# Optimization experiments

Measured on AMD Instinct MI355X. Metric: run time of the kernel, lower is better.

The kernel has to match this reference:

```python
import jax, jax.numpy as jnp
import numpy as np

DIM = 768
HEADS = 12
N_PATCH = 1024
ORDER = 5
DECAY = 0.5
EPS = 1e-6


def _exact_mask(N, order, decay):
    # 2D grid graph adjacency, row-major node order (matches sorted nx.grid_2d_graph nodes)
    side = int(np.sqrt(N))
    A = np.zeros((N, N), dtype=np.float64)
    idx = np.arange(N)
    r, c = idx // side, idx % side
    right = idx[c < side - 1]
    A[right, right + 1] = 1.0
    A[right + 1, right] = 1.0
    down = idx[r < side - 1]
    A[down, down + side] = 1.0
    A[down + side, down] = 1.0
    D_inv = 1.0 / np.maximum(A.sum(axis=1), 1.0)
    W = D_inv[:, None] * A
    M = np.eye(N)
    W_k = np.eye(N)
    coeff = 1.0
    for _ in range(order):
        W_k = W_k @ W
        coeff *= decay
        M += coeff * W_k
    M = M / M.sum(axis=1, keepdims=True)
    return jnp.asarray(M, dtype=jnp.float32)


def setup_inputs() -> dict:
    key = jax.random.key(0)
    k1, k2, k3, k4 = jax.random.split(key, 4)
    B = 4
    x = jax.random.normal(k1, (B, N_PATCH, DIM), dtype=jnp.float32)
    # nn.Linear(dim, 3*dim, bias=False): store as [dim, 3*dim] for x @ W
    scale = 1.0 / np.sqrt(DIM)
    W_qkv = jax.random.uniform(k2, (DIM, 3 * DIM), dtype=jnp.float32, minval=-scale, maxval=scale)
    W_out = jax.random.uniform(k3, (DIM, DIM), dtype=jnp.float32, minval=-scale, maxval=scale)
    b_out = jax.random.uniform(k4, (DIM,), dtype=jnp.float32, minval=-scale, maxval=scale)
    mask = _exact_mask(N_PATCH, ORDER, DECAY)
    return {"x": x, "W_qkv": W_qkv, "W_out": W_out, "b_out": b_out, "mask": mask}


def reference(x, W_qkv, W_out, b_out, mask):
    B, N, C = x.shape
    H, D = HEADS, C // HEADS
    qkv = x @ W_qkv  # [B, N, 3C]
    q, k, v = jnp.split(qkv, 3, axis=-1)
    # [B, N, C] -> [B, H, N, D]
    q, k, v = (t.reshape(B, N, H, D).transpose(0, 2, 1, 3) for t in (q, k, v))
    # feature map
    q = jax.nn.relu(q) + EPS
    k = jax.nn.relu(k) + EPS
    # (q^T @ M)^T = M^T @ q  ->  einsum over node axis
    q_graph = jnp.einsum('nm,bhnd->bhmd', mask, q)
    k_graph = jnp.einsum('nm,bhnd->bhmd', mask, k)
    q = q + 0.1 * q_graph
    k = k + 0.1 * k_graph
    linear_kernel = jnp.einsum('bhnd,bhmd->bhnm', q, k)  # [B, H, N, N]
    masked_kernel = linear_kernel * mask[None, None, :, :]
    z = 1.0 / (masked_kernel.sum(axis=-1, keepdims=True) + EPS)  # [B, H, N, 1]
    out = jnp.einsum('bhnm,bhmd->bhnd', masked_kernel, v) * z
    out = out.transpose(0, 2, 1, 3).reshape(B, N, C)
    return out @ W_out + b_out
```

## Files before the change

### kernel.cpp

```cpp
#include <hip/hip_runtime.h>

#define NP   1024
#define DIM  768
#define NH   12
#define HD   64
#define TQ   2304
#define EPS  1e-6f

typedef __attribute__((ext_vector_type(8))) short bf16x8;
typedef __attribute__((ext_vector_type(4))) float f32x4;

#define MFMA(a, b, c) __builtin_amdgcn_mfma_f32_16x16x32_bf16((a), (b), (c), 0, 0, 0)

__device__ __forceinline__ unsigned short f2b(float x) {
    unsigned int u = __builtin_bit_cast(unsigned int, x);
    u = (u + 0x7fffu + ((u >> 16) & 1u)) >> 16;
    return (unsigned short)u;
}
__device__ __forceinline__ float b2f(unsigned short h) {
    unsigned int u = ((unsigned int)h) << 16;
    return __builtin_bit_cast(float, u);
}
#if __has_builtin(__builtin_amdgcn_cvt_pk_bf16_f32)
typedef __attribute__((ext_vector_type(2))) __bf16 bf16x2t;
__device__ __forceinline__ unsigned int pk2(float lo, float hi) {
    bf16x2t v = __builtin_amdgcn_cvt_pk_bf16_f32(lo, hi);
    return __builtin_bit_cast(unsigned int, v);
}
#else
__device__ __forceinline__ unsigned int pk2(float lo, float hi) {
    return (unsigned int)f2b(lo) | ((unsigned int)f2b(hi) << 16);
}
#endif
__device__ __forceinline__ void gld16(const void* g, void* l) {
    __builtin_amdgcn_global_load_lds((const __attribute__((address_space(1))) unsigned int*)g,
                                     (__attribute__((address_space(3))) unsigned int*)l,
                                     16, 0, 0);
}

__global__ __launch_bounds__(256) void k_prep(const float* __restrict__ W_qkv,
                                              const float* __restrict__ W_out,
                                              const float* __restrict__ mask,
                                              unsigned short* __restrict__ WqkvT,
                                              unsigned short* __restrict__ WoutT,
                                              unsigned short* __restrict__ M2) {
    __shared__ float buf[64][65];
    const int bx = blockIdx.x, t = threadIdx.x;
    const float* in; unsigned short* outp; int R, C, ct, rt; bool isMask = false;
    if (bx < 432)      { int q = bx;       in = W_qkv; outp = WqkvT; R = 768;  C = 2304; ct = q % 36; rt = q / 36; }
    else if (bx < 576) { int q = bx - 432; in = W_out; outp = WoutT; R = 768;  C = 768;  ct = q % 12; rt = q / 12; }
    else               { int q = bx - 576; in = mask;  outp = M2;    R = 1024; C = 1024; ct = q % 16; rt = q / 16; isMask = true; }
    const int r0 = rt * 64, c0 = ct * 64;
    const int rr = t >> 4, cc = (t & 15) * 4;
    #pragma unroll
    for (int p = 0; p < 4; ++p) {
        float4 v = *(const float4*)(in + (size_t)(r0 + p * 16 + rr) * C + c0 + cc);
        buf[p * 16 + rr][cc + 0] = v.x; buf[p * 16 + rr][cc + 1] = v.y;
        buf[p * 16 + rr][cc + 2] = v.z; buf[p * 16 + rr][cc + 3] = v.w;
    }
    __syncthreads();
    const int oc = t >> 2, orr = (t & 3) * 16;
    alignas(16) unsigned short tmp[16];
    if (isMask) {
        #pragma unroll
        for (int j = 0; j < 16; ++j) {
            float v = 0.1f * buf[orr + j][oc] + ((c0 + oc) == (r0 + orr + j) ? 1.f : 0.f);
            tmp[j] = f2b(v);
        }
    } else {
        #pragma unroll
        for (int j = 0; j < 16; ++j) tmp[j] = f2b(buf[orr + j][oc]);
    }
    unsigned short* dst = outp + (size_t)(c0 + oc) * R + r0 + orr;
    *(uint4*)dst = *(const uint4*)tmp;
    *(uint4*)(dst + 8) = *(const uint4*)(tmp + 8);
}

__global__ __launch_bounds__(512) void k_gemm1(const float* __restrict__ X,
                                               const unsigned short* __restrict__ Bt,
                                               unsigned short* __restrict__ T) {
    __shared__ unsigned short As[2][128][32];
    __shared__ unsigned short Bs[2][128][32];
    const int tid = threadIdx.x, w = tid >> 6, l = tid & 63;
    const int bid = blockIdx.x;
    const int mstrip = (bid & 7) * 4 + ((bid >> 3) & 3);
    const int nstrip = bid >> 5;
    const int m0 = mstrip * 128, n0 = nstrip * 128;
    const int wm = (w & 3) * 32, wn = (w >> 2) * 64;
    const int quad = l >> 4, col = l & 15;
    const int lr = l >> 2, lc = (l & 3) * 8;
    const int arow = tid >> 2, akc = (tid & 3) * 8;

    f32x4 acc[2][4] = {};
    for (int k0 = 0; k0 < DIM; k0 += 64) {
        #pragma unroll
        for (int hh = 0; hh < 2; ++hh) {
            gld16(Bt + (size_t)(n0 + w * 16 + lr) * DIM + k0 + hh * 32 + lc, &Bs[hh][w * 16][0]);
            const float* xp = X + (size_t)(m0 + arow) * DIM + k0 + hh * 32 + akc;
            float4 xa = *(const float4*)xp;
            float4 xb = *(const float4*)(xp + 4);
            uint4 o;
            o.x = pk2(xa.x, xa.y); o.y = pk2(xa.z, xa.w);
            o.z = pk2(xb.x, xb.y); o.w = pk2(xb.z, xb.w);
            *(uint4*)&As[hh][arow][akc] = o;
        }
        __syncthreads();
        #pragma unroll
        for (int hh = 0; hh < 2; ++hh) {
            bf16x8 a[2], b[4];
            #pragma unroll
            for (int i = 0; i < 2; ++i) a[i] = *(const bf16x8*)&As[hh][wm + i * 16 + col][quad * 8];
            #pragma unroll
            for (int j = 0; j < 4; ++j) b[j] = *(const bf16x8*)&Bs[hh][wn + j * 16 + col][quad * 8];
            #pragma unroll
            for (int i = 0; i < 2; ++i)
                #pragma unroll
                for (int j = 0; j < 4; ++j)
                    acc[i][j] = MFMA(a[i], b[j], acc[i][j]);
        }
        __syncthreads();
    }

    const int cgb = n0 + wn;
    const int slot = cgb / DIM;
    const int h = (cgb % DIM) >> 6;
    const bool act = (slot < 2);
    const int sh = slot * 48 + (m0 >> 10) * NH + h;
    const int npb = (m0 & 1023) + wm + quad * 4;
    #pragma unroll
    for (int j = 0; j < 4; ++j) {
        unsigned short* dcol = T + ((size_t)(sh * HD + j * 16 + col)) * NP + npb;
        #pragma unroll
        for (int i = 0; i < 2; ++i) {
            float v0 = acc[i][j][0], v1 = acc[i][j][1], v2 = acc[i][j][2], v3 = acc[i][j][3];
            if (act) {
                v0 = fmaxf(v0, 0.f) + EPS; v1 = fmaxf(v1, 0.f) + EPS;
                v2 = fmaxf(v2, 0.f) + EPS; v3 = fmaxf(v3, 0.f) + EPS;
            }
            uint2 o; o.x = pk2(v0, v1); o.y = pk2(v2, v3);
            *(uint2*)(dcol + i * 16) = o;
        }
    }
}

__global__ __launch_bounds__(256) void k_graphmix(const unsigned short* __restrict__ M2,
                                                  const unsigned short* __restrict__ T,
                                                  unsigned short* __restrict__ q2) {
    const int bh = blockIdx.y, mt = blockIdx.x;
    const int m0 = mt * 64;
    __shared__ unsigned short M2s[4][64][32], Fq[4][64][32], Fk[4][64][32];
    const int tid = threadIdx.x, w = tid >> 6, l = tid & 63;
    const int quad = l >> 4, col = l & 15;
    const int lr = l >> 2, lc = (l & 3) * 8;
    const unsigned short* Tq = T + (size_t)bh * HD * NP;
    const unsigned short* Tk = T + (size_t)(48 + bh) * HD * NP;

    f32x4 accq[4] = {}, acck[4] = {};
    const int nr0 = min(max(2 * mt - 5, 0), 20) * 32;
    for (int it = 0; it < 3; ++it) {
        const int nc = nr0 + it * 128;
        __syncthreads();
        #pragma unroll
        for (int hh = 0; hh < 4; ++hh) {
            gld16(M2 + (size_t)(m0 + w * 16 + lr) * NP + nc + hh * 32 + lc, &M2s[hh][w * 16][0]);
            gld16(Tq + (size_t)(w * 16 + lr) * NP + nc + hh * 32 + lc, &Fq[hh][w * 16][0]);
            gld16(Tk + (size_t)(w * 16 + lr) * NP + nc + hh * 32 + lc, &Fk[hh][w * 16][0]);
        }
        __syncthreads();
        #pragma unroll
        for (int ks = 0; ks < 4; ++ks) {
            bf16x8 bm = *(const bf16x8*)&M2s[ks][w * 16 + col][quad * 8];
            #pragma unroll
            for (int dt = 0; dt < 4; ++dt) {
                bf16x8 aq = *(const bf16x8*)&Fq[ks][dt * 16 + col][quad * 8];
                bf16x8 ak = *(const bf16x8*)&Fk[ks][dt * 16 + col][quad * 8];
                accq[dt] = MFMA(aq, bm, accq[dt]);
                acck[dt] = MFMA(ak, bm, acck[dt]);
            }
        }
    }
    unsigned short* q2q = q2 + ((size_t)bh * NP + m0 + w * 16 + col) * HD;
    unsigned short* q2k = q2 + ((size_t)(48 + bh) * NP + m0 + w * 16 + col) * HD;
    #pragma unroll
    for (int dt = 0; dt < 4; ++dt) {
        const int d0 = dt * 16 + quad * 4;
        uint2 oq; oq.x = pk2(accq[dt][0], accq[dt][1]); oq.y = pk2(accq[dt][2], accq[dt][3]);
        uint2 ok; ok.x = pk2(acck[dt][0], acck[dt][1]); ok.y = pk2(acck[dt][2], acck[dt][3]);
        *(uint2*)(q2q + d0) = oq;
        *(uint2*)(q2k + d0) = ok;
    }
}

__global__ __launch_bounds__(256) void k_attn(const unsigned short* __restrict__ q2,
                                              const unsigned short* __restrict__ T,
                                              const float* __restrict__ mask,
                                              unsigned short* __restrict__ attnb) {
    const int bh = blockIdx.y, b = bh / NH, h = bh % NH;
    const int nt = blockIdx.x, n0 = nt * 64;
    __shared__ unsigned short Qs[2][64][32];
    __shared__ unsigned short Ks[2][64][32];
    __shared__ unsigned short VT[2][64][32];
    __shared__ unsigned int Ss2[32][68];
    __shared__ float rowz[64];
    const int tid = threadIdx.x, w = tid >> 6, l = tid & 63;
    const int quad = l >> 4, col = l & 15;
    const int lr = l >> 2, lc = (l & 3) * 8;

    const unsigned short* qb = q2 + ((size_t)bh * NP + n0) * HD;
    const unsigned short* kb = q2 + (size_t)(48 + bh) * NP * HD;
    const unsigned short* vtb = T + (size_t)(96 + bh) * HD * NP;

    #pragma unroll
    for (int hh = 0; hh < 2; ++hh)
        gld16(qb + (size_t)(w * 16 + lr) * HD + hh * 32 + lc, &Qs[hh][w * 16][0]);

    f32x4 oacc[4] = {};
    float racc[4] = {};
    const int mr0 = min(max(2 * nt - 5, 0), 20) * 32;
    const unsigned int sel = (col & 1) ? 0x07060302u : 0x05040100u;

    for (int it = 0; it < 6; ++it) {
        const int m0 = mr0 + it * 64;
        __syncthreads();
        #pragma unroll
        for (int hh = 0; hh < 2; ++hh) {
            gld16(kb + (size_t)(m0 + w * 16 + lr) * HD + hh * 32 + lc, &Ks[hh][w * 16][0]);
            gld16(vtb + (size_t)(w * 16 + lr) * NP + m0 + hh * 32 + lc, &VT[hh][w * 16][0]);
        }
        float mreg[4][4];
        #pragma unroll
        for (int mtt = 0; mtt < 4; ++mtt)
            #pragma unroll
            for (int r = 0; r < 4; ++r)
                mreg[mtt][r] = mask[(size_t)(n0 + w * 16 + quad * 4 + r) * NP
                                    + m0 + mtt * 16 + col];
        __syncthreads();

        f32x4 s[4] = {};
        #pragma unroll
        for (int ks = 0; ks < 2; ++ks) {
            bf16x8 aq = *(const bf16x8*)&Qs[ks][w * 16 + col][quad * 8];
            #pragma unroll
            for (int mtt = 0; mtt < 4; ++mtt) {
                bf16x8 bk = *(const bf16x8*)&Ks[ks][mtt * 16 + col][quad * 8];
                s[mtt] = MFMA(aq, bk, s[mtt]);
            }
        }
        {
            const int npr = w * 8 + quad * 2;
            #pragma unroll
            for (int mtt = 0; mtt < 4; ++mtt) {
                float v0 = s[mtt][0] * mreg[mtt][0];
                float v1 = s[mtt][1] * mreg[mtt][1];
                float v2 = s[mtt][2] * mreg[mtt][2];
                float v3 = s[mtt][3] * mreg[mtt][3];
                racc[0] += v0; racc[1] += v1; racc[2] += v2; racc[3] += v3;
                Ss2[npr][mtt * 16 + col]     = pk2(v0, v1);
                Ss2[npr + 1][mtt * 16 + col] = pk2(v2, v3);
            }
        }
        __syncthreads();
        #pragma unroll
        for (int ks = 0; ks < 2; ++ks) {
            const unsigned int* rp = &Ss2[w * 8 + (col >> 1)][ks * 32 + quad * 8];
            uint4 U  = *(const uint4*)rp;
            uint4 U2 = *(const uint4*)(rp + 4);
            uint4 fr;
            fr.x = __builtin_amdgcn_perm(U.y,  U.x,  sel);
            fr.y = __builtin_amdgcn_perm(U.w,  U.z,  sel);
            fr.z = __builtin_amdgcn_perm(U2.y, U2.x, sel);
            fr.w = __builtin_amdgcn_perm(U2.w, U2.z, sel);
            bf16x8 as = __builtin_bit_cast(bf16x8, fr);
            #pragma unroll
            for (int dt = 0; dt < 4; ++dt) {
                bf16x8 bv = *(const bf16x8*)&VT[ks][dt * 16 + col][quad * 8];
                oacc[dt] = MFMA(as, bv, oacc[dt]);
            }
        }
    }

    #pragma unroll
    for (int r = 0; r < 4; ++r) {
        float v = racc[r];
        v += __shfl_xor(v, 1); v += __shfl_xor(v, 2);
        v += __shfl_xor(v, 4); v += __shfl_xor(v, 8);
        if (col == 0) rowz[w * 16 + quad * 4 + r] = v;
    }
    __syncthreads();
    #pragma unroll
    for (int r = 0; r < 4; ++r) {
        const int nl = w * 16 + quad * 4 + r;
        const float z = 1.f / (rowz[nl] + EPS);
        #pragma unroll
        for (int dt = 0; dt < 4; ++dt)
            attnb[(size_t)(b * NP + n0 + nl) * DIM + h * HD + dt * 16 + col] =
                f2b(oacc[dt][r] * z);
    }
}

__global__ __launch_bounds__(256) void k_gemm2(const unsigned short* __restrict__ A,
                                               const unsigned short* __restrict__ Bt,
                                               const float* __restrict__ bias,
                                               float* __restrict__ C) {
    __shared__ unsigned short As[2][64][32];
    __shared__ unsigned short Bs[2][64][32];
    const int tid = threadIdx.x, w = tid >> 6, l = tid & 63;
    const int bid = blockIdx.x;
    const int mstrip = (bid & 7) * 8 + ((bid >> 3) & 7);
    const int nstrip = bid >> 6;
    const int m0 = mstrip * 64, n0 = nstrip * 64;
    const int wm = (w & 1) * 32, wn = (w >> 1) * 32;
    const int quad = l >> 4, col = l & 15;
    const int lr = l >> 2, lc = (l & 3) * 8;

    f32x4 acc[2][2] = {};
    for (int k0 = 0; k0 < DIM; k0 += 64) {
        #pragma unroll
        for (int hh = 0; hh < 2; ++hh) {
            gld16(A + (size_t)(m0 + w * 16 + lr) * DIM + k0 + hh * 32 + lc, &As[hh][w * 16][0]);
            gld16(Bt + (size_t)(n0 + w * 16 + lr) * DIM + k0 + hh * 32 + lc, &Bs[hh][w * 16][0]);
        }
        __syncthreads();
        #pragma unroll
        for (int hh = 0; hh < 2; ++hh) {
            bf16x8 a[2], b[2];
            #pragma unroll
            for (int i = 0; i < 2; ++i) a[i] = *(const bf16x8*)&As[hh][wm + i * 16 + col][quad * 8];
            #pragma unroll
            for (int j = 0; j < 2; ++j) b[j] = *(const bf16x8*)&Bs[hh][wn + j * 16 + col][quad * 8];
            #pragma unroll
            for (int i = 0; i < 2; ++i)
                #pragma unroll
                for (int j = 0; j < 2; ++j)
                    acc[i][j] = MFMA(a[i], b[j], acc[i][j]);
        }
        __syncthreads();
    }
    #pragma unroll
    for (int i = 0; i < 2; ++i)
        #pragma unroll
        for (int j = 0; j < 2; ++j) {
            const int n = n0 + wn + j * 16 + col;
            #pragma unroll
            for (int r = 0; r < 4; ++r) {
                const int m = m0 + wm + i * 16 + quad * 4 + r;
                C[(size_t)m * DIM + n] = acc[i][j][r] + bias[n];
            }
        }
}

extern "C" void kernel_launch(void* const* d_in, const int* in_sizes, int n_in,
                              void* d_out, int out_size, void* d_ws, size_t ws_size,
                              hipStream_t stream) {
    (void)in_sizes; (void)n_in; (void)out_size; (void)ws_size;
    const float* x     = (const float*)d_in[0];
    const float* W_qkv = (const float*)d_in[1];
    const float* W_out = (const float*)d_in[2];
    const float* b_out = (const float*)d_in[3];
    const float* mask  = (const float*)d_in[4];
    float* out = (float*)d_out;

    unsigned short* p = (unsigned short*)d_ws;
    unsigned short* WqkvT = p; p += (size_t)TQ * DIM;
    unsigned short* WoutT = p; p += (size_t)DIM * DIM;
    unsigned short* M2    = p; p += (size_t)NP * NP;
    unsigned short* T     = p; p += (size_t)3 * 48 * HD * NP;
    unsigned short* q2    = p; p += (size_t)2 * 48 * NP * HD;
    unsigned short* attnb = p; p += (size_t)4096 * DIM;

    k_prep<<<dim3(832), 256, 0, stream>>>(W_qkv, W_out, mask, WqkvT, WoutT, M2);
    k_gemm1<<<dim3(576), 512, 0, stream>>>(x, WqkvT, T);
    k_graphmix<<<dim3(NP / 64, 48), 256, 0, stream>>>(M2, T, q2);
    k_attn<<<dim3(NP / 64, 48), 256, 0, stream>>>(q2, T, mask, attnb);
    k_gemm2<<<dim3(768), 256, 0, stream>>>(attnb, WoutT, b_out, out);
}
```

Measured before the change: 156.8 us.

## Load MFMA operands directly from global memory in graphmix and attention kernels

In the graph-mix kernel, the M2 operand is now read straight from global memory into registers instead of being staged through shared memory. In the attention kernel, the Q, K and V^T MFMA fragments are loaded directly from global memory into registers. This drops the LDS staging and most barriers, and the score buffer is double-buffered so only one barrier per iteration remains. The output GEMM's K step grows from 64 to 128 to halve its barrier count. The trade-off is more register pressure and uncoalesced per-lane global loads in exchange for fewer LDS round trips and syncs.

```diff
diff --git a/kernel.cpp b/kernel.cpp
--- a/kernel.cpp
+++ b/kernel.cpp
@@ -148,12 +148,13 @@
                                                   unsigned short* __restrict__ q2) {
     const int bh = blockIdx.y, mt = blockIdx.x;
     const int m0 = mt * 64;
-    __shared__ unsigned short M2s[4][64][32], Fq[4][64][32], Fk[4][64][32];
+    __shared__ unsigned short Fq[4][64][32], Fk[4][64][32];
     const int tid = threadIdx.x, w = tid >> 6, l = tid & 63;
     const int quad = l >> 4, col = l & 15;
     const int lr = l >> 2, lc = (l & 3) * 8;
     const unsigned short* Tq = T + (size_t)bh * HD * NP;
     const unsigned short* Tk = T + (size_t)(48 + bh) * HD * NP;
+    const unsigned short* mrow = M2 + (size_t)(m0 + w * 16 + col) * NP;
 
     f32x4 accq[4] = {}, acck[4] = {};
     const int nr0 = min(max(2 * mt - 5, 0), 20) * 32;
@@ -162,22 +163,23 @@
         __syncthreads();
         #pragma unroll
         for (int hh = 0; hh < 4; ++hh) {
-            gld16(M2 + (size_t)(m0 + w * 16 + lr) * NP + nc + hh * 32 + lc, &M2s[hh][w * 16][0]);
             gld16(Tq + (size_t)(w * 16 + lr) * NP + nc + hh * 32 + lc, &Fq[hh][w * 16][0]);
             gld16(Tk + (size_t)(w * 16 + lr) * NP + nc + hh * 32 + lc, &Fk[hh][w * 16][0]);
         }
-        __syncthreads();
-        #pragma unroll
-        for (int ks = 0; ks < 4; ++ks) {
-            bf16x8 bm = *(const bf16x8*)&M2s[ks][w * 16 + col][quad * 8];
+        bf16x8 bm[4];
+        #pragma unroll
+        for (int ks = 0; ks < 4; ++ks)
+            bm[ks] = *(const bf16x8*)(mrow + nc + ks * 32 + quad * 8);
+        __syncthreads();
+        #pragma unroll
+        for (int ks = 0; ks < 4; ++ks)
             #pragma unroll
             for (int dt = 0; dt < 4; ++dt) {
                 bf16x8 aq = *(const bf16x8*)&Fq[ks][dt * 16 + col][quad * 8];
                 bf16x8 ak = *(const bf16x8*)&Fk[ks][dt * 16 + col][quad * 8];
-                accq[dt] = MFMA(aq, bm, accq[dt]);
-                acck[dt] = MFMA(ak, bm, acck[dt]);
+                accq[dt] = MFMA(aq, bm[ks], accq[dt]);
+                acck[dt] = MFMA(ak, bm[ks], acck[dt]);
             }
-        }
     }
     unsigned short* q2q = q2 + ((size_t)bh * NP + m0 + w * 16 + col) * HD;
     unsigned short* q2k = q2 + ((size_t)(48 + bh) * NP + m0 + w * 16 + col) * HD;
@@ -197,36 +199,43 @@
                                               unsigned short* __restrict__ attnb) {
     const int bh = blockIdx.y, b = bh / NH, h = bh % NH;
     const int nt = blockIdx.x, n0 = nt * 64;
-    __shared__ unsigned short Qs[2][64][32];
-    __shared__ unsigned short Ks[2][64][32];
-    __shared__ unsigned short VT[2][64][32];
-    __shared__ unsigned int Ss2[32][68];
+    __shared__ unsigned int Ss2[2][32][68];
     __shared__ float rowz[64];
     const int tid = threadIdx.x, w = tid >> 6, l = tid & 63;
     const int quad = l >> 4, col = l & 15;
-    const int lr = l >> 2, lc = (l & 3) * 8;
 
     const unsigned short* qb = q2 + ((size_t)bh * NP + n0) * HD;
     const unsigned short* kb = q2 + (size_t)(48 + bh) * NP * HD;
     const unsigned short* vtb = T + (size_t)(96 + bh) * HD * NP;
 
-    #pragma unroll
-    for (int hh = 0; hh < 2; ++hh)
-        gld16(qb + (size_t)(w * 16 + lr) * HD + hh * 32 + lc, &Qs[hh][w * 16][0]);
+    bf16x8 aq[2];
+    #pragma unroll
+    for (int ks = 0; ks < 2; ++ks)
+        aq[ks] = *(const bf16x8*)(qb + (size_t)(w * 16 + col) * HD + ks * 32 + quad * 8);
 
     f32x4 oacc[4] = {};
     float racc[4] = {};
     const int mr0 = min(max(2 * nt - 5, 0), 20) * 32;
     const unsigned int sel = (col & 1) ? 0x07060302u : 0x05040100u;
 
+    #pragma unroll
     for (int it = 0; it < 6; ++it) {
         const int m0 = mr0 + it * 64;
-        __syncthreads();
-        #pragma unroll
-        for (int hh = 0; hh < 2; ++hh) {
-            gld16(kb + (size_t)(m0 + w * 16 + lr) * HD + hh * 32 + lc, &Ks[hh][w * 16][0]);
-            gld16(vtb + (size_t)(w * 16 + lr) * NP + m0 + hh * 32 + lc, &VT[hh][w * 16][0]);
-        }
+        const int pp = it & 1;
+        bf16x8 bv[2][4];
+        #pragma unroll
+        for (int ks = 0; ks < 2; ++ks)
+            #pragma unroll
+            for (int dt = 0; dt < 4; ++dt)
+                bv[ks][dt] = *(const bf16x8*)(vtb + (size_t)(dt * 16 + col) * NP
+                                              + m0 + ks * 32 + quad * 8);
+        bf16x8 bk[2][4];
+        #pragma unroll
+        for (int ks = 0; ks < 2; ++ks)
+            #pragma unroll
+            for (int mtt = 0; mtt < 4; ++mtt)
+                bk[ks][mtt] = *(const bf16x8*)(kb + (size_t)(m0 + mtt * 16 + col) * HD
+                                               + ks * 32 + quad * 8);
         float mreg[4][4];
         #pragma unroll
         for (int mtt = 0; mtt < 4; ++mtt)
@@ -234,18 +243,12 @@
             for (int r = 0; r < 4; ++r)
                 mreg[mtt][r] = mask[(size_t)(n0 + w * 16 + quad * 4 + r) * NP
                                     + m0 + mtt * 16 + col];
-        __syncthreads();
-
         f32x4 s[4] = {};
         #pragma unroll
-        for (int ks = 0; ks < 2; ++ks) {
-            bf16x8 aq = *(const bf16x8*)&Qs[ks][w * 16 + col][quad * 8];
-            #pragma unroll
-            for (int mtt = 0; mtt < 4; ++mtt) {
-                bf16x8 bk = *(const bf16x8*)&Ks[ks][mtt * 16 + col][quad * 8];
-                s[mtt] = MFMA(aq, bk, s[mtt]);
-            }
-        }
+        for (int ks = 0; ks < 2; ++ks)
+            #pragma unroll
+            for (int mtt = 0; mtt < 4; ++mtt)
+                s[mtt] = MFMA(aq[ks], bk[ks][mtt], s[mtt]);
         {
             const int npr = w * 8 + quad * 2;
             #pragma unroll
@@ -255,14 +258,14 @@
                 float v2 = s[mtt][2] * mreg[mtt][2];
                 float v3 = s[mtt][3] * mreg[mtt][3];
                 racc[0] += v0; racc[1] += v1; racc[2] += v2; racc[3] += v3;
-                Ss2[npr][mtt * 16 + col]     = pk2(v0, v1);
-                Ss2[npr + 1][mtt * 16 + col] = pk2(v2, v3);
+                Ss2[pp][npr][mtt * 16 + col]     = pk2(v0, v1);
+                Ss2[pp][npr + 1][mtt * 16 + col] = pk2(v2, v3);
             }
         }
         __syncthreads();
         #pragma unroll
         for (int ks = 0; ks < 2; ++ks) {
-            const unsigned int* rp = &Ss2[w * 8 + (col >> 1)][ks * 32 + quad * 8];
+            const unsigned int* rp = &Ss2[pp][w * 8 + (col >> 1)][ks * 32 + quad * 8];
             uint4 U  = *(const uint4*)rp;
             uint4 U2 = *(const uint4*)(rp + 4);
             uint4 fr;
@@ -272,10 +275,8 @@
             fr.w = __builtin_amdgcn_perm(U2.w, U2.z, sel);
             bf16x8 as = __builtin_bit_cast(bf16x8, fr);
             #pragma unroll
-            for (int dt = 0; dt < 4; ++dt) {
-                bf16x8 bv = *(const bf16x8*)&VT[ks][dt * 16 + col][quad * 8];
-                oacc[dt] = MFMA(as, bv, oacc[dt]);
-            }
+            for (int dt = 0; dt < 4; ++dt)
+                oacc[dt] = MFMA(as, bv[ks][dt], oacc[dt]);
         }
     }
 
@@ -302,8 +303,8 @@
                                                const unsigned short* __restrict__ Bt,
                                                const float* __restrict__ bias,
                                                float* __restrict__ C) {
-    __shared__ unsigned short As[2][64][32];
-    __shared__ unsigned short Bs[2][64][32];
+    __shared__ unsigned short As[4][64][32];
+    __shared__ unsigned short Bs[4][64][32];
     const int tid = threadIdx.x, w = tid >> 6, l = tid & 63;
     const int bid = blockIdx.x;
     const int mstrip = (bid & 7) * 8 + ((bid >> 3) & 7);
@@ -314,15 +315,15 @@
     const int lr = l >> 2, lc = (l & 3) * 8;
 
     f32x4 acc[2][2] = {};
-    for (int k0 = 0; k0 < DIM; k0 += 64) {
-        #pragma unroll
-        for (int hh = 0; hh < 2; ++hh) {
+    for (int k0 = 0; k0 < DIM; k0 += 128) {
+        #pragma unroll
+        for (int hh = 0; hh < 4; ++hh) {
             gld16(A + (size_t)(m0 + w * 16 + lr) * DIM + k0 + hh * 32 + lc, &As[hh][w * 16][0]);
             gld16(Bt + (size_t)(n0 + w * 16 + lr) * DIM + k0 + hh * 32 + lc, &Bs[hh][w * 16][0]);
         }
         __syncthreads();
         #pragma unroll
-        for (int hh = 0; hh < 2; ++hh) {
+        for (int hh = 0; hh < 4; ++hh) {
             bf16x8 a[2], b[2];
             #pragma unroll
             for (int i = 0; i < 2; ++i) a[i] = *(const bf16x8*)&As[hh][wm + i * 16 + col][quad * 8];
```

After: 178.7 us. +14.0%, slower.

## Overlap W_out/mask prep with QKV GEMM and double attention tile per sync

Applied to the files above, without the earlier changes.

The prep kernel is split so only the W_qkv transpose runs before the QKV GEMM. The W_out and mask transposes become extra blocks appended to the GEMM launch, each using two 256-thread halves, so they can overlap with GEMM work. The attention kernel now loads Q fragments straight into registers, drops the Q shared-memory tile, and processes two 64-wide K/V tiles per barrier round, halving the number of syncs. The cost is more shared memory and registers in k_attn, which may lower occupancy. The transpose buffer pitch also changes from 65 to 68.

```diff
diff --git a/kernel.cpp b/kernel.cpp
--- a/kernel.cpp
+++ b/kernel.cpp
@@ -38,25 +38,17 @@
                                      16, 0, 0);
 }
 
-__global__ __launch_bounds__(256) void k_prep(const float* __restrict__ W_qkv,
-                                              const float* __restrict__ W_out,
-                                              const float* __restrict__ mask,
-                                              unsigned short* __restrict__ WqkvT,
-                                              unsigned short* __restrict__ WoutT,
-                                              unsigned short* __restrict__ M2) {
-    __shared__ float buf[64][65];
-    const int bx = blockIdx.x, t = threadIdx.x;
-    const float* in; unsigned short* outp; int R, C, ct, rt; bool isMask = false;
-    if (bx < 432)      { int q = bx;       in = W_qkv; outp = WqkvT; R = 768;  C = 2304; ct = q % 36; rt = q / 36; }
-    else if (bx < 576) { int q = bx - 432; in = W_out; outp = WoutT; R = 768;  C = 768;  ct = q % 12; rt = q / 12; }
-    else               { int q = bx - 576; in = mask;  outp = M2;    R = 1024; C = 1024; ct = q % 16; rt = q / 16; isMask = true; }
+__device__ __forceinline__ void tile_transpose(const float* in, unsigned short* outp,
+                                               int R, int C, int rt, int ct,
+                                               bool isMask, float* buf ,
+                                               int t ) {
     const int r0 = rt * 64, c0 = ct * 64;
     const int rr = t >> 4, cc = (t & 15) * 4;
     #pragma unroll
     for (int p = 0; p < 4; ++p) {
         float4 v = *(const float4*)(in + (size_t)(r0 + p * 16 + rr) * C + c0 + cc);
-        buf[p * 16 + rr][cc + 0] = v.x; buf[p * 16 + rr][cc + 1] = v.y;
-        buf[p * 16 + rr][cc + 2] = v.z; buf[p * 16 + rr][cc + 3] = v.w;
+        buf[(p * 16 + rr) * 68 + cc + 0] = v.x; buf[(p * 16 + rr) * 68 + cc + 1] = v.y;
+        buf[(p * 16 + rr) * 68 + cc + 2] = v.z; buf[(p * 16 + rr) * 68 + cc + 3] = v.w;
     }
     __syncthreads();
     const int oc = t >> 2, orr = (t & 3) * 16;
@@ -64,25 +56,48 @@
     if (isMask) {
         #pragma unroll
         for (int j = 0; j < 16; ++j) {
-            float v = 0.1f * buf[orr + j][oc] + ((c0 + oc) == (r0 + orr + j) ? 1.f : 0.f);
+            float v = 0.1f * buf[(orr + j) * 68 + oc] + ((c0 + oc) == (r0 + orr + j) ? 1.f : 0.f);
             tmp[j] = f2b(v);
         }
     } else {
         #pragma unroll
-        for (int j = 0; j < 16; ++j) tmp[j] = f2b(buf[orr + j][oc]);
+        for (int j = 0; j < 16; ++j) tmp[j] = f2b(buf[(orr + j) * 68 + oc]);
     }
     unsigned short* dst = outp + (size_t)(c0 + oc) * R + r0 + orr;
     *(uint4*)dst = *(const uint4*)tmp;
     *(uint4*)(dst + 8) = *(const uint4*)(tmp + 8);
 }
 
+__global__ __launch_bounds__(256) void k_prep1(const float* __restrict__ W_qkv,
+                                               unsigned short* __restrict__ WqkvT) {
+    __shared__ float buf[64 * 68];
+    tile_transpose(W_qkv, WqkvT, 768, 2304, blockIdx.x / 36, blockIdx.x % 36,
+                   false, buf, threadIdx.x);
+}
+
 __global__ __launch_bounds__(512) void k_gemm1(const float* __restrict__ X,
                                                const unsigned short* __restrict__ Bt,
-                                               unsigned short* __restrict__ T) {
-    __shared__ unsigned short As[2][128][32];
-    __shared__ unsigned short Bs[2][128][32];
-    const int tid = threadIdx.x, w = tid >> 6, l = tid & 63;
+                                               unsigned short* __restrict__ T,
+                                               const float* __restrict__ W_out,
+                                               const float* __restrict__ mask,
+                                               unsigned short* __restrict__ WoutT,
+                                               unsigned short* __restrict__ M2) {
+    __shared__ __align__(16) unsigned char smem[34816];
+    const int tid = threadIdx.x;
     const int bid = blockIdx.x;
+
+    if (bid >= 576) {
+        const int job = (bid - 576) * 2 + (tid >> 8);
+        float* buf = (float*)(smem + (tid >> 8) * 17408);
+        const int tt = tid & 255;
+        if (job < 144) tile_transpose(W_out, WoutT, 768, 768, job / 12, job % 12, false, buf, tt);
+        else { int j = job - 144; tile_transpose(mask, M2, 1024, 1024, j / 16, j % 16, true, buf, tt); }
+        return;
+    }
+
+    unsigned short* As = (unsigned short*)smem;
+    unsigned short* Bs = As + 2 * 128 * 32;
+    const int w = tid >> 6, l = tid & 63;
     const int mstrip = (bid & 7) * 4 + ((bid >> 3) & 3);
     const int nstrip = bid >> 5;
     const int m0 = mstrip * 128, n0 = nstrip * 128;
@@ -95,23 +110,26 @@
     for (int k0 = 0; k0 < DIM; k0 += 64) {
         #pragma unroll
         for (int hh = 0; hh < 2; ++hh) {
-            gld16(Bt + (size_t)(n0 + w * 16 + lr) * DIM + k0 + hh * 32 + lc, &Bs[hh][w * 16][0]);
+            gld16(Bt + (size_t)(n0 + w * 16 + lr) * DIM + k0 + hh * 32 + lc,
+                  Bs + (hh * 128 + w * 16) * 32);
             const float* xp = X + (size_t)(m0 + arow) * DIM + k0 + hh * 32 + akc;
             float4 xa = *(const float4*)xp;
             float4 xb = *(const float4*)(xp + 4);
             uint4 o;
             o.x = pk2(xa.x, xa.y); o.y = pk2(xa.z, xa.w);
             o.z = pk2(xb.x, xb.y); o.w = pk2(xb.z, xb.w);
-            *(uint4*)&As[hh][arow][akc] = o;
+            *(uint4*)(As + (hh * 128 + arow) * 32 + akc) = o;
         }
         __syncthreads();
         #pragma unroll
         for (int hh = 0; hh < 2; ++hh) {
             bf16x8 a[2], b[4];
             #pragma unroll
-            for (int i = 0; i < 2; ++i) a[i] = *(const bf16x8*)&As[hh][wm + i * 16 + col][quad * 8];
-            #pragma unroll
-            for (int j = 0; j < 4; ++j) b[j] = *(const bf16x8*)&Bs[hh][wn + j * 16 + col][quad * 8];
+            for (int i = 0; i < 2; ++i)
+                a[i] = *(const bf16x8*)(As + (hh * 128 + wm + i * 16 + col) * 32 + quad * 8);
+            #pragma unroll
+            for (int j = 0; j < 4; ++j)
+                b[j] = *(const bf16x8*)(Bs + (hh * 128 + wn + j * 16 + col) * 32 + quad * 8);
             #pragma unroll
             for (int i = 0; i < 2; ++i)
                 #pragma unroll
@@ -197,10 +215,9 @@
                                               unsigned short* __restrict__ attnb) {
     const int bh = blockIdx.y, b = bh / NH, h = bh % NH;
     const int nt = blockIdx.x, n0 = nt * 64;
-    __shared__ unsigned short Qs[2][64][32];
-    __shared__ unsigned short Ks[2][64][32];
-    __shared__ unsigned short VT[2][64][32];
-    __shared__ unsigned int Ss2[32][68];
+    __shared__ unsigned short Ks[2][2][64][32];
+    __shared__ unsigned short VT[2][2][64][32];
+    __shared__ unsigned int Ss2[2][32][68];
     __shared__ float rowz[64];
     const int tid = threadIdx.x, w = tid >> 6, l = tid & 63;
     const int quad = l >> 4, col = l & 15;
@@ -210,73 +227,82 @@
     const unsigned short* kb = q2 + (size_t)(48 + bh) * NP * HD;
     const unsigned short* vtb = T + (size_t)(96 + bh) * HD * NP;
 
-    #pragma unroll
-    for (int hh = 0; hh < 2; ++hh)
-        gld16(qb + (size_t)(w * 16 + lr) * HD + hh * 32 + lc, &Qs[hh][w * 16][0]);
+    bf16x8 aq[2];
+    #pragma unroll
+    for (int ks = 0; ks < 2; ++ks)
+        aq[ks] = *(const bf16x8*)(qb + (size_t)(w * 16 + col) * HD + ks * 32 + quad * 8);
 
     f32x4 oacc[4] = {};
     float racc[4] = {};
     const int mr0 = min(max(2 * nt - 5, 0), 20) * 32;
     const unsigned int sel = (col & 1) ? 0x07060302u : 0x05040100u;
 
-    for (int it = 0; it < 6; ++it) {
-        const int m0 = mr0 + it * 64;
-        __syncthreads();
-        #pragma unroll
-        for (int hh = 0; hh < 2; ++hh) {
-            gld16(kb + (size_t)(m0 + w * 16 + lr) * HD + hh * 32 + lc, &Ks[hh][w * 16][0]);
-            gld16(vtb + (size_t)(w * 16 + lr) * NP + m0 + hh * 32 + lc, &VT[hh][w * 16][0]);
-        }
-        float mreg[4][4];
-        #pragma unroll
-        for (int mtt = 0; mtt < 4; ++mtt)
-            #pragma unroll
-            for (int r = 0; r < 4; ++r)
-                mreg[mtt][r] = mask[(size_t)(n0 + w * 16 + quad * 4 + r) * NP
-                                    + m0 + mtt * 16 + col];
-        __syncthreads();
-
-        f32x4 s[4] = {};
-        #pragma unroll
-        for (int ks = 0; ks < 2; ++ks) {
-            bf16x8 aq = *(const bf16x8*)&Qs[ks][w * 16 + col][quad * 8];
+    for (int it3 = 0; it3 < 3; ++it3) {
+        const int m0a = mr0 + it3 * 128;
+        __syncthreads();
+        #pragma unroll
+        for (int t2 = 0; t2 < 2; ++t2)
+            #pragma unroll
+            for (int hh = 0; hh < 2; ++hh) {
+                gld16(kb + (size_t)(m0a + t2 * 64 + w * 16 + lr) * HD + hh * 32 + lc,
+                      &Ks[t2][hh][w * 16][0]);
+                gld16(vtb + (size_t)(w * 16 + lr) * NP + m0a + t2 * 64 + hh * 32 + lc,
+                      &VT[t2][hh][w * 16][0]);
+            }
+        float mreg[2][4][4];
+        #pragma unroll
+        for (int t2 = 0; t2 < 2; ++t2)
+            #pragma unroll
+            for (int mtt = 0; mtt < 4; ++mtt)
+                #pragma unroll
+                for (int r = 0; r < 4; ++r)
+                    mreg[t2][mtt][r] = mask[(size_t)(n0 + w * 16 + quad * 4 + r) * NP
+                                            + m0a + t2 * 64 + mtt * 16 + col];
+        __syncthreads();
+
+        #pragma unroll
+        for (int t2 = 0; t2 < 2; ++t2) {
+            f32x4 s[4] = {};
+            #pragma unroll
+            for (int ks = 0; ks < 2; ++ks)
+                #pragma unroll
+                for (int mtt = 0; mtt < 4; ++mtt) {
+                    bf16x8 bk = *(const bf16x8*)&Ks[t2][ks][mtt * 16 + col][quad * 8];
+                    s[mtt] = MFMA(aq[ks], bk, s[mtt]);
+                }
+            const int npr = w * 8 + quad * 2;
             #pragma unroll
             for (int mtt = 0; mtt < 4; ++mtt) {
-                bf16x8 bk = *(const bf16x8*)&Ks[ks][mtt * 16 + col][quad * 8];
-                s[mtt] = MFMA(aq, bk, s[mtt]);
-            }
-        }
-        {
-            const int npr = w * 8 + quad * 2;
-            #pragma unroll
-            for (int mtt = 0; mtt < 4; ++mtt) {
-                float v0 = s[mtt][0] * mreg[mtt][0];
-                float v1 = s[mtt][1] * mreg[mtt][1];
-                float v2 = s[mtt][2] * mreg[mtt][2];
-                float v3 = s[mtt][3] * mreg[mtt][3];
+                float v0 = s[mtt][0] * mreg[t2][mtt][0];
+                float v1 = s[mtt][1] * mreg[t2][mtt][1];
+                float v2 = s[mtt][2] * mreg[t2][mtt][2];
+                float v3 = s[mtt][3] * mreg[t2][mtt][3];
                 racc[0] += v0; racc[1] += v1; racc[2] += v2; racc[3] += v3;
-                Ss2[npr][mtt * 16 + col]     = pk2(v0, v1);
-                Ss2[npr + 1][mtt * 16 + col] = pk2(v2, v3);
-            }
-        }
-        __syncthreads();
-        #pragma unroll
-        for (int ks = 0; ks < 2; ++ks) {
-            const unsigned int* rp = &Ss2[w * 8 + (col >> 1)][ks * 32 + quad * 8];
-            uint4 U  = *(const uint4*)rp;
-            uint4 U2 = *(const uint4*)(rp + 4);
-            uint4 fr;
-            fr.x = __builtin_amdgcn_perm(U.y,  U.x,  sel);
-            fr.y = __builtin_amdgcn_perm(U.w,  U.z,  sel);
-            fr.z = __builtin_amdgcn_perm(U2.y, U2.x, sel);
-            fr.w = __builtin_amdgcn_perm(U2.w, U2.z, sel);
-            bf16x8 as = __builtin_bit_cast(bf16x8, fr);
-            #pragma unroll
-            for (int dt = 0; dt < 4; ++dt) {
-                bf16x8 bv = *(const bf16x8*)&VT[ks][dt * 16 + col][quad * 8];
-                oacc[dt] = MFMA(as, bv, oacc[dt]);
-            }
-        }
+                Ss2[t2][npr][mtt * 16 + col]     = pk2(v0, v1);
+                Ss2[t2][npr + 1][mtt * 16 + col] = pk2(v2, v3);
+            }
+        }
+        __syncthreads();
+
+        #pragma unroll
+        for (int t2 = 0; t2 < 2; ++t2)
+            #pragma unroll
+            for (int ks = 0; ks < 2; ++ks) {
+                const unsigned int* rp = &Ss2[t2][w * 8 + (col >> 1)][ks * 32 + quad * 8];
+                uint4 U  = *(const uint4*)rp;
+                uint4 U2 = *(const uint4*)(rp + 4);
+                uint4 fr;
+                fr.x = __builtin_amdgcn_perm(U.y,  U.x,  sel);
+                fr.y = __builtin_amdgcn_perm(U.w,  U.z,  sel);
+                fr.z = __builtin_amdgcn_perm(U2.y, U2.x, sel);
+                fr.w = __builtin_amdgcn_perm(U2.w, U2.z, sel);
+                bf16x8 as = __builtin_bit_cast(bf16x8, fr);
+                #pragma unroll
+                for (int dt = 0; dt < 4; ++dt) {
+                    bf16x8 bv = *(const bf16x8*)&VT[t2][ks][dt * 16 + col][quad * 8];
+                    oacc[dt] = MFMA(as, bv, oacc[dt]);
+                }
+            }
     }
 
     #pragma unroll
@@ -368,8 +394,8 @@
     unsigned short* q2    = p; p += (size_t)2 * 48 * NP * HD;
     unsigned short* attnb = p; p += (size_t)4096 * DIM;
 
-    k_prep<<<dim3(832), 256, 0, stream>>>(W_qkv, W_out, mask, WqkvT, WoutT, M2);
-    k_gemm1<<<dim3(576), 512, 0, stream>>>(x, WqkvT, T);
+    k_prep1<<<dim3(432), 256, 0, stream>>>(W_qkv, WqkvT);
+    k_gemm1<<<dim3(776), 512, 0, stream>>>(x, WqkvT, T, W_out, mask, WoutT, M2);
     k_graphmix<<<dim3(NP / 64, 48), 256, 0, stream>>>(M2, T, q2);
     k_attn<<<dim3(NP / 64, 48), 256, 0, stream>>>(q2, T, mask, attnb);
     k_gemm2<<<dim3(768), 256, 0, stream>>>(attnb, WoutT, b_out, out);
```

Measured after the change: 155.0 us. About the same (-1.2%).
